# Optimization experiments

Hardware: AMD Instinct MI355X
Metric: run time of the kernel (lower is better)

## Reference

```python
import jax, jax.numpy as jnp
import numpy as np

N_ATOMS = 200000   # total atoms in batch
N_NBR   = 10       # max neighbors per atom (a2a width)
N_MOLS  = 8000     # molecules in batch (25 atoms each)
HID     = 128      # hidden_size
FDIM    = 151      # raw atom feature dim (GROVER default)
FEAT    = 200      # molecule-level descriptor dim
DFF     = 4 * HID  # PositionwiseFeedForward inner dim
FFN_H   = 256      # mol_atom_from_atom_ffn hidden
TASKS   = 12       # num_tasks
EPS     = 1e-6     # GROVER LayerNorm eps


def setup_inputs() -> dict:
    key = jax.random.key(0)
    ks = jax.random.split(key, 14)
    s = 0.02
    atoms_per_mol = N_ATOMS // N_MOLS
    starts = (jnp.arange(N_MOLS, dtype=jnp.int32) * atoms_per_mol)
    sizes = jnp.full((N_MOLS,), atoms_per_mol, dtype=jnp.int32)
    a_scope = jnp.stack([starts, sizes], axis=1)  # [M, 2]
    return {
        "atom_output": jax.random.normal(ks[0], (N_ATOMS, HID), jnp.float32),
        "original_f_atoms": jax.random.normal(ks[1], (N_ATOMS, FDIM), jnp.float32),
        "features_batch": jax.random.normal(ks[2], (N_MOLS, FEAT), jnp.float32),
        "a2a": jax.random.randint(ks[3], (N_ATOMS, N_NBR), 0, N_ATOMS, jnp.int32),
        "a_scope": a_scope,
        # PositionwiseFeedForward (ffn_atom_from_atom): in = FDIM + HID
        "W1": jax.random.normal(ks[4], (FDIM + HID, DFF), jnp.float32) * s,
        "b1": jnp.zeros((DFF,), jnp.float32),
        "W2": jax.random.normal(ks[5], (DFF, HID), jnp.float32) * s,
        "b2": jnp.zeros((HID,), jnp.float32),
        # SublayerConnection LayerNorm
        "gamma": jnp.ones((HID,), jnp.float32),
        "beta": jnp.zeros((HID,), jnp.float32),
        # mol_atom_from_atom_ffn: in = HID + FEAT
        "Wf1": jax.random.normal(ks[6], (HID + FEAT, FFN_H), jnp.float32) * s,
        "bf1": jnp.zeros((FFN_H,), jnp.float32),
        "Wf2": jax.random.normal(ks[7], (FFN_H, TASKS), jnp.float32) * s,
        "bf2": jnp.zeros((TASKS,), jnp.float32),
    }


def _layernorm(x, gamma, beta):
    mu = jnp.mean(x, axis=-1, keepdims=True)
    var = jnp.mean((x - mu) ** 2, axis=-1, keepdims=True)
    return gamma * (x - mu) * jax.lax.rsqrt(var + EPS) + beta


def reference(atom_output, original_f_atoms, features_batch, a2a, a_scope,
              W1, b1, W2, b2, gamma, beta, Wf1, bf1, Wf2, bf2):
    # select_neighbor_and_aggregate: gather neighbor embeddings, sum over nbrs
    aggr = jnp.sum(atom_output[a2a], axis=1)                      # [N, HID]
    x = jnp.concatenate([original_f_atoms, aggr], axis=1)         # [N, FDIM+HID]
    # PositionwiseFeedForward (eval: dropout = identity)
    h = jax.nn.relu(x @ W1 + b1)
    ffn_out = h @ W2 + b2                                         # [N, HID]
    # SublayerConnection(None, x) -> dropout(LayerNorm(x))
    atom_emb = _layernorm(ffn_out, gamma, beta)                   # [N, HID]
    # Readout: mean-pool per molecule via a_scope (start, size)
    starts = a_scope[:, 0]
    sizes = a_scope[:, 1].astype(atom_emb.dtype)
    seg = jnp.searchsorted(starts, jnp.arange(atom_emb.shape[0], dtype=starts.dtype), side="right") - 1
    mol = jax.ops.segment_sum(atom_emb, seg, num_segments=a_scope.shape[0]) / sizes[:, None]
    # concat molecule descriptors, then mol_atom_from_atom_ffn
    mol = jnp.concatenate([mol, features_batch], axis=1)          # [M, HID+FEAT]
    out = jax.nn.relu(mol @ Wf1 + bf1) @ Wf2 + bf2                # [M, TASKS]
    return out
```

## Files before the change

kernel.cpp:

```cpp
#include <hip/hip_runtime.h>
#include <hip/hip_bf16.h>

#define N_ATOMS 200000
#define N_NBR 10
#define N_MOLS 8000
#define HID 128
#define FDIM 151
#define FEAT 200
#define DFF 512
#define FFN_H 256
#define TASKS 12
#define KX 279
#define K1P 288
#define XS 296
#define HSTR 136
#define FS 132
#define KM 328
#define K3 352
#define MS 360
#define MT 80
#define MI 5
#define NCHUNK 4
#define SMEM_ATOMS (MT * XS * 2 + MT * HSTR * 2)

typedef __hip_bfloat16 bf16;
typedef __attribute__((ext_vector_type(8))) __bf16 bf16x8;
typedef __attribute__((ext_vector_type(4))) float f32x4;

__device__ __forceinline__ float bf2f(bf16 x) { return __bfloat162float(x); }
__device__ __forceinline__ float blo(unsigned w) { union { unsigned u; float f; } c; c.u = w << 16; return c.f; }
__device__ __forceinline__ float bhi(unsigned w) { union { unsigned u; float f; } c; c.u = w & 0xFFFF0000u; return c.f; }

__global__ void prep_weights_kernel(const float* __restrict__ W1,
                                    const float* __restrict__ W2,
                                    const float* __restrict__ Wf1,
                                    bf16* __restrict__ W1bT,
                                    bf16* __restrict__ W2bT,
                                    bf16* __restrict__ Wf1bT) {
  int idx = blockIdx.x * 256 + threadIdx.x;
  if (idx < DFF * K1P) {
    int n = idx / K1P, k = idx - n * K1P;
    float v;
    if (k < HID)      v = W1[(size_t)(FDIM + k) * DFF + n];
    else if (k < KX)  v = W1[(size_t)(k - HID) * DFF + n];
    else              v = 0.f;
    W1bT[idx] = __float2bfloat16(v);
    return;
  }
  idx -= DFF * K1P;
  if (idx < HID * DFF) {
    int n = idx / DFF, k = idx - n * DFF;
    W2bT[idx] = __float2bfloat16(W2[(size_t)k * HID + n]);
    return;
  }
  idx -= HID * DFF;
  if (idx < FFN_H * K3) {
    int n = idx / K3, k = idx - n * K3;
    float v = (k < KM) ? Wf1[(size_t)k * FFN_H + n] : 0.f;
    Wf1bT[idx] = __float2bfloat16(v);
  }
}

__global__ void conv_ao_kernel(const float* __restrict__ ao, bf16* __restrict__ ao16) {
  const int idx = blockIdx.x * 256 + threadIdx.x;
  const float4 v0 = *(const float4*)&ao[(size_t)idx * 8];
  const float4 v1 = *(const float4*)&ao[(size_t)idx * 8 + 4];
  union { bf16 h[8]; uint4 u; } pk;
  pk.h[0] = __float2bfloat16(v0.x); pk.h[1] = __float2bfloat16(v0.y);
  pk.h[2] = __float2bfloat16(v0.z); pk.h[3] = __float2bfloat16(v0.w);
  pk.h[4] = __float2bfloat16(v1.x); pk.h[5] = __float2bfloat16(v1.y);
  pk.h[6] = __float2bfloat16(v1.z); pk.h[7] = __float2bfloat16(v1.w);
  *(uint4*)&ao16[(size_t)idx * 8] = pk.u;
}

__global__ __launch_bounds__(256)
void gather_kernel(const bf16* __restrict__ ao16,
                   const int* __restrict__ a2a,
                   bf16* __restrict__ aggr) {
  const int gid = blockIdx.x * 256 + threadIdx.x;
  const int atom = gid >> 4, c8 = gid & 15;
  int idxs[N_NBR];
#pragma unroll
  for (int j = 0; j < N_NBR; ++j) idxs[j] = a2a[atom * N_NBR + j];
  float s[8];
#pragma unroll
  for (int e = 0; e < 8; ++e) s[e] = 0.f;
#pragma unroll
  for (int j = 0; j < N_NBR; ++j) {
    const uint4 u = *(const uint4*)&ao16[(size_t)idxs[j] * HID + c8 * 8];
    s[0] += blo(u.x); s[1] += bhi(u.x);
    s[2] += blo(u.y); s[3] += bhi(u.y);
    s[4] += blo(u.z); s[5] += bhi(u.z);
    s[6] += blo(u.w); s[7] += bhi(u.w);
  }
  union { bf16 h[8]; uint4 u; } pk;
#pragma unroll
  for (int e = 0; e < 8; ++e) pk.h[e] = __float2bfloat16(s[e]);
  *(uint4*)&aggr[(size_t)atom * HID + c8 * 8] = pk.u;
}

__global__ __launch_bounds__(512, 4)
void atoms_kernel(const bf16* __restrict__ aggr,
                  const float* __restrict__ f_atoms,
                  const bf16* __restrict__ W1bT,
                  const float* __restrict__ b1,
                  const bf16* __restrict__ W2bT,
                  const float* __restrict__ b2,
                  const float* __restrict__ gamma,
                  const float* __restrict__ beta,
                  bf16* __restrict__ atom_emb) {
  extern __shared__ char smem[];
  bf16* Xs = (bf16*)smem;
  bf16* Hs = (bf16*)(smem + MT * XS * 2);
  float* Fs = (float*)smem;

  const int tid = threadIdx.x;
  const int m0 = blockIdx.x * MT;
  const int lane = tid & 63;
  const int w = tid >> 6;
  const int lr = lane & 15;
  const int lk = lane >> 4;

  const float4 b2v = *(const float4*)&b2[w * 16 + lk * 4];
  const float gam0 = gamma[lane], gam1 = gamma[64 + lane];
  const float bet0 = beta[lane],  bet1 = beta[64 + lane];

  {
    int q = tid;
#pragma unroll
    for (int p = 0; p < 3; ++p) {
      if (p < 2 || q < MT * 16) {
        const int r = q >> 4, c8 = q & 15;
        *(uint4*)&Xs[r * XS + c8 * 8] = *(const uint4*)&aggr[(size_t)(m0 + r) * HID + c8 * 8];
      }
      q += 512;
    }
  }
  {
    const float* fb = &f_atoms[(size_t)m0 * FDIM];
    int q = tid;
#pragma unroll
    for (int p = 0; p < 6; ++p) {
      if (p < 5 || q < (MT * FDIM) / 4) {
        const float4 v = *(const float4*)&fb[q * 4];
        const float vf[4] = { v.x, v.y, v.z, v.w };
        const int flat = q * 4;
        const int r0 = flat / FDIM, c0 = flat - r0 * FDIM;
#pragma unroll
        for (int e = 0; e < 4; ++e) {
          const int cc = c0 + e;
          const int off = (cc < FDIM) ? (r0 * XS + HID + cc) : ((r0 + 1) * XS + HID + cc - FDIM);
          Xs[off] = __float2bfloat16(vf[e]);
        }
      }
      q += 512;
    }
  }
  {
    int q = tid;
#pragma unroll
    for (int p = 0; p < 2; ++p) {
      if (q < MT * (K1P - KX)) {
        const int r = q / (K1P - KX), cc = q - r * (K1P - KX);
        Xs[r * XS + KX + cc] = __float2bfloat16(0.f);
      }
      q += 512;
    }
  }
  __syncthreads();

  f32x4 acc2[MI];
#pragma unroll
  for (int mi = 0; mi < MI; ++mi) acc2[mi] = (f32x4)0.f;

#pragma unroll 1
  for (int nc = 0; nc < NCHUNK; ++nc) {
    f32x4 acc1[MI];
#pragma unroll
    for (int mi = 0; mi < MI; ++mi) acc1[mi] = (f32x4)0.f;
    const bf16* w1row = &W1bT[(size_t)(nc * 128 + w * 16 + lr) * K1P + lk * 8];
    __builtin_amdgcn_s_setprio(1);
#pragma unroll
    for (int kk = 0; kk < K1P / 32; ++kk) {
      const bf16x8 b = *(const bf16x8*)&w1row[kk * 32];
#pragma unroll
      for (int mi = 0; mi < MI; ++mi) {
        const bf16x8 a = *(const bf16x8*)&Xs[(mi * 16 + lr) * XS + kk * 32 + lk * 8];
        acc1[mi] = __builtin_amdgcn_mfma_f32_16x16x32_bf16(b, a, acc1[mi], 0, 0, 0);
      }
    }
    __builtin_amdgcn_s_setprio(0);
    {
      const float4 bb = *(const float4*)&b1[nc * 128 + w * 16 + lk * 4];
      const float bbf[4] = { bb.x, bb.y, bb.z, bb.w };
      const int nb4 = w * 16 + lk * 4;
#pragma unroll
      for (int mi = 0; mi < MI; ++mi) {
        union { bf16 h[4]; uint2 u2; } pk;
#pragma unroll
        for (int r = 0; r < 4; ++r) {
          const float h = acc1[mi][r] + bbf[r];
          pk.h[r] = __float2bfloat16(h > 0.f ? h : 0.f);
        }
        *(uint2*)&Hs[(mi * 16 + lr) * HSTR + nb4] = pk.u2;
      }
    }
    __syncthreads();

    const bf16* w2row = &W2bT[(size_t)(w * 16 + lr) * DFF + nc * 128 + lk * 8];
    __builtin_amdgcn_s_setprio(1);
#pragma unroll
    for (int kk = 0; kk < 4; ++kk) {
      const bf16x8 b = *(const bf16x8*)&w2row[kk * 32];
#pragma unroll
      for (int mi = 0; mi < MI; ++mi) {
        const bf16x8 a = *(const bf16x8*)&Hs[(mi * 16 + lr) * HSTR + kk * 32 + lk * 8];
        acc2[mi] = __builtin_amdgcn_mfma_f32_16x16x32_bf16(b, a, acc2[mi], 0, 0, 0);
      }
    }
    __builtin_amdgcn_s_setprio(0);
    if (nc < NCHUNK - 1) __syncthreads();
  }

  {
    const int nb4 = w * 16 + lk * 4;
#pragma unroll
    for (int mi = 0; mi < MI; ++mi) {
      float4 v;
      v.x = acc2[mi][0] + b2v.x;
      v.y = acc2[mi][1] + b2v.y;
      v.z = acc2[mi][2] + b2v.z;
      v.w = acc2[mi][3] + b2v.w;
      *(float4*)&Fs[(mi * 16 + lr) * FS + nb4] = v;
    }
  }
  __syncthreads();

#pragma unroll
  for (int i = 0; i < MT / 8; ++i) {
    const int row = w * (MT / 8) + i;
    const float x0 = Fs[row * FS + lane];
    const float x1 = Fs[row * FS + 64 + lane];
    float s = x0 + x1;
    float q = x0 * x0 + x1 * x1;
#pragma unroll
    for (int off = 32; off > 0; off >>= 1) {
      s += __shfl_xor(s, off);
      q += __shfl_xor(q, off);
    }
    const float mu = s * (1.f / 128.f);
    const float var = q * (1.f / 128.f) - mu * mu;
    const float rs = rsqrtf(var + 1e-6f);
    const int atom = m0 + row;
    atom_emb[(size_t)atom * HID + lane] =
        __float2bfloat16(gam0 * ((x0 - mu) * rs) + bet0);
    atom_emb[(size_t)atom * HID + 64 + lane] =
        __float2bfloat16(gam1 * ((x1 - mu) * rs) + bet1);
  }
}

__global__ __launch_bounds__(256)
void mol_kernel(const bf16* __restrict__ atom_emb,
                const float* __restrict__ features,
                const int* __restrict__ a_scope,
                bf16* __restrict__ mol_cat) {
  const int tid = threadIdx.x;
  const int mi = tid >> 4, c8 = tid & 15;
  const int base = blockIdx.x * 16;
  const int m = base + mi;
  const int start = a_scope[2 * m];
  const int size  = a_scope[2 * m + 1];
  float s[8];
#pragma unroll
  for (int e = 0; e < 8; ++e) s[e] = 0.f;
  for (int a = 0; a < size; ++a) {
    const uint4 u = *(const uint4*)&atom_emb[(size_t)(start + a) * HID + c8 * 8];
    s[0] += blo(u.x); s[1] += bhi(u.x);
    s[2] += blo(u.y); s[3] += bhi(u.y);
    s[4] += blo(u.z); s[5] += bhi(u.z);
    s[6] += blo(u.w); s[7] += bhi(u.w);
  }
  const float inv = 1.f / (float)size;
  union { bf16 h[8]; uint4 u; } pk;
#pragma unroll
  for (int e = 0; e < 8; ++e) pk.h[e] = __float2bfloat16(s[e] * inv);
  *(uint4*)&mol_cat[(size_t)m * K3 + c8 * 8] = pk.u;
  for (int q = tid; q < 16 * 50; q += 256) {
    const int mm = q / 50, qq = q - mm * 50;
    const float4 v = *(const float4*)&features[(size_t)(base + mm) * FEAT + qq * 4];
    union { bf16 h[4]; uint2 u2; } pf;
    pf.h[0] = __float2bfloat16(v.x); pf.h[1] = __float2bfloat16(v.y);
    pf.h[2] = __float2bfloat16(v.z); pf.h[3] = __float2bfloat16(v.w);
    *(uint2*)&mol_cat[(size_t)(base + mm) * K3 + HID + qq * 4] = pf.u2;
  }
  for (int q = tid; q < 16 * (K3 - KM); q += 256) {
    const int mm = q / (K3 - KM), qq = q - mm * (K3 - KM);
    mol_cat[(size_t)(base + mm) * K3 + KM + qq] = __float2bfloat16(0.f);
  }
}

__global__ __launch_bounds__(512)
void molffn1_kernel(const bf16* __restrict__ mol_cat,
                    const bf16* __restrict__ Wf1bT,
                    const float* __restrict__ bf1,
                    bf16* __restrict__ Hf) {
  __shared__ bf16 As[64 * MS];
  const int tid = threadIdx.x;
  const int m0 = blockIdx.x * 64;
  for (int idx = tid; idx < 64 * (K3 / 8); idx += 512) {
    int rr = idx / (K3 / 8), qv = idx - rr * (K3 / 8);
    *(uint4*)&As[rr * MS + qv * 8] = *(const uint4*)&mol_cat[(size_t)(m0 + rr) * K3 + qv * 8];
  }
  __syncthreads();
  const int lane = tid & 63, w = tid >> 6;
  const int lr = lane & 15, lk = lane >> 4;
  const int wn = w * 32;
  f32x4 acc[4][2];
#pragma unroll
  for (int mi = 0; mi < 4; ++mi)
#pragma unroll
    for (int ni = 0; ni < 2; ++ni) acc[mi][ni] = (f32x4)0.f;
#pragma unroll 3
  for (int kk = 0; kk < K3 / 32; ++kk) {
    bf16x8 a[4], b[2];
#pragma unroll
    for (int mi = 0; mi < 4; ++mi)
      a[mi] = *(const bf16x8*)&As[(mi * 16 + lr) * MS + kk * 32 + lk * 8];
#pragma unroll
    for (int ni = 0; ni < 2; ++ni)
      b[ni] = *(const bf16x8*)&Wf1bT[(size_t)(wn + ni * 16 + lr) * K3 + kk * 32 + lk * 8];
#pragma unroll
    for (int mi = 0; mi < 4; ++mi)
#pragma unroll
      for (int ni = 0; ni < 2; ++ni)
        acc[mi][ni] = __builtin_amdgcn_mfma_f32_16x16x32_bf16(a[mi], b[ni], acc[mi][ni], 0, 0, 0);
  }
#pragma unroll
  for (int ni = 0; ni < 2; ++ni) {
    const int n = wn + ni * 16 + lr;
    const float bias = bf1[n];
#pragma unroll
    for (int mi = 0; mi < 4; ++mi)
#pragma unroll
      for (int rr = 0; rr < 4; ++rr) {
        const int row = mi * 16 + lk * 4 + rr;
        const float h = acc[mi][ni][rr] + bias;
        Hf[(size_t)(m0 + row) * FFN_H + n] = __float2bfloat16(h > 0.f ? h : 0.f);
      }
  }
}

__global__ __launch_bounds__(192)
void molffn2_kernel(const bf16* __restrict__ Hf,
                    const float* __restrict__ Wf2,
                    const float* __restrict__ bias2,
                    float* __restrict__ out) {
  __shared__ float Ws[FFN_H * TASKS];
  const int tid = threadIdx.x;
  for (int i = tid; i < FFN_H * TASKS; i += 192) Ws[i] = Wf2[i];
  __syncthreads();
  const int m = blockIdx.x * 16 + tid / TASKS;
  const int t = tid % TASKS;
  float s = bias2[t];
  for (int k8 = 0; k8 < FFN_H / 8; ++k8) {
    const uint4 u = *(const uint4*)&Hf[(size_t)m * FFN_H + k8 * 8];
    const float h[8] = { blo(u.x), bhi(u.x), blo(u.y), bhi(u.y),
                         blo(u.z), bhi(u.z), blo(u.w), bhi(u.w) };
#pragma unroll
    for (int e = 0; e < 8; ++e) s += h[e] * Ws[(k8 * 8 + e) * TASKS + t];
  }
  out[(size_t)m * TASKS + t] = s;
}

extern "C" void kernel_launch(void* const* d_in, const int* in_sizes, int n_in,
                              void* d_out, int out_size, void* d_ws, size_t ws_size,
                              hipStream_t stream) {
  const float* atom_output = (const float*)d_in[0];
  const float* f_atoms     = (const float*)d_in[1];
  const float* features    = (const float*)d_in[2];
  const int*   a2a         = (const int*)d_in[3];
  const int*   a_scope     = (const int*)d_in[4];
  const float* W1   = (const float*)d_in[5];
  const float* b1   = (const float*)d_in[6];
  const float* W2   = (const float*)d_in[7];
  const float* b2   = (const float*)d_in[8];
  const float* gamma = (const float*)d_in[9];
  const float* beta  = (const float*)d_in[10];
  const float* Wf1  = (const float*)d_in[11];
  const float* bf1  = (const float*)d_in[12];
  const float* Wf2  = (const float*)d_in[13];
  const float* bf2v = (const float*)d_in[14];
  float* out = (float*)d_out;

  char* ws = (char*)d_ws;
  size_t off = 0;
  bf16* W1bT  = (bf16*)(ws + off); off += (size_t)DFF * K1P * 2;
  bf16* W2bT  = (bf16*)(ws + off); off += (size_t)HID * DFF * 2;
  bf16* Wf1bT = (bf16*)(ws + off); off += (size_t)FFN_H * K3 * 2;
  bf16* atom_emb = (bf16*)(ws + off); off += (size_t)N_ATOMS * HID * 2;
  bf16* mol_cat  = (bf16*)(ws + off); off += (size_t)N_MOLS * K3 * 2;
  bf16* Hf       = (bf16*)(ws + off); off += (size_t)N_MOLS * FFN_H * 2;
  bf16* ao16     = (bf16*)(ws + off); off += (size_t)N_ATOMS * HID * 2;
  bf16* aggr = atom_emb;

  static int smem_set = 0;
  (void)smem_set;
  hipFuncSetAttribute((const void*)atoms_kernel,
                      hipFuncAttributeMaxDynamicSharedMemorySize, SMEM_ATOMS);

  hipLaunchKernelGGL(prep_weights_kernel, dim3(1184), dim3(256), 0, stream,
                     W1, W2, Wf1, W1bT, W2bT, Wf1bT);
  hipLaunchKernelGGL(conv_ao_kernel, dim3(N_ATOMS * HID / 8 / 256), dim3(256), 0, stream,
                     atom_output, ao16);
  hipLaunchKernelGGL(gather_kernel, dim3(N_ATOMS * 16 / 256), dim3(256), 0, stream,
                     ao16, a2a, aggr);
  hipLaunchKernelGGL(atoms_kernel, dim3(N_ATOMS / MT), dim3(512), SMEM_ATOMS, stream,
                     aggr, f_atoms,
                     W1bT, b1, W2bT, b2, gamma, beta, atom_emb);
  hipLaunchKernelGGL(mol_kernel, dim3(N_MOLS / 16), dim3(256), 0, stream,
                     atom_emb, features, a_scope, mol_cat);
  hipLaunchKernelGGL(molffn1_kernel, dim3(N_MOLS / 64), dim3(512), 0, stream,
                     mol_cat, Wf1bT, bf1, Hf);
  hipLaunchKernelGGL(molffn2_kernel, dim3(N_MOLS / 16), dim3(192), 0, stream,
                     Hf, Wf2, bf2v, out);
}
```

Measured before the change: 285.6 us.

## Retile atom FFN kernel to 2x4 warp tiles with 64-row blocks

Changes the fused atom FFN kernel from 80-row tiles, where each warp owns a 16-column strip across all rows, to 64-row tiles with a 2x4 warp grid. Each warp now computes a 32x64 block of the first GEMM and a 32x32 block of the second GEMM, processing DFF in two 256-wide chunks instead of four 128-wide chunks. The aim is more register-level reuse of A and B fragments (several MFMAs per load), fewer weight reloads from global memory, and fewer barriers. In exchange the kernel uses more accumulator registers, which may lower occupancy, and launches more blocks because each block covers fewer rows.

```diff
diff --git a/kernel.cpp b/kernel.cpp
--- a/kernel.cpp
+++ b/kernel.cpp
@@ -13,15 +13,14 @@
 #define KX 279
 #define K1P 288
 #define XS 296
-#define HSTR 136
+#define HS2 264
 #define FS 132
 #define KM 328
 #define K3 352
 #define MS 360
-#define MT 80
-#define MI 5
-#define NCHUNK 4
-#define SMEM_ATOMS (MT * XS * 2 + MT * HSTR * 2)
+#define MT 64
+#define NC 256
+#define SMEM_ATOMS (MT * XS * 2 + MT * HS2 * 2)
 
 typedef __hip_bfloat16 bf16;
 typedef __attribute__((ext_vector_type(8))) __bf16 bf16x8;
@@ -120,19 +119,18 @@
   const int w = tid >> 6;
   const int lr = lane & 15;
   const int lk = lane >> 4;
-
-  const float4 b2v = *(const float4*)&b2[w * 16 + lk * 4];
+  const int wm = w & 1;
+  const int wq = w >> 1;
+
   const float gam0 = gamma[lane], gam1 = gamma[64 + lane];
   const float bet0 = beta[lane],  bet1 = beta[64 + lane];
 
   {
     int q = tid;
 #pragma unroll
-    for (int p = 0; p < 3; ++p) {
-      if (p < 2 || q < MT * 16) {
-        const int r = q >> 4, c8 = q & 15;
-        *(uint4*)&Xs[r * XS + c8 * 8] = *(const uint4*)&aggr[(size_t)(m0 + r) * HID + c8 * 8];
-      }
+    for (int p = 0; p < 2; ++p) {
+      const int r = q >> 4, c8 = q & 15;
+      *(uint4*)&Xs[r * XS + c8 * 8] = *(const uint4*)&aggr[(size_t)(m0 + r) * HID + c8 * 8];
       q += 512;
     }
   }
@@ -140,8 +138,8 @@
     const float* fb = &f_atoms[(size_t)m0 * FDIM];
     int q = tid;
 #pragma unroll
-    for (int p = 0; p < 6; ++p) {
-      if (p < 5 || q < (MT * FDIM) / 4) {
+    for (int p = 0; p < 5; ++p) {
+      if (p < 4 || q < (MT * FDIM) / 4) {
         const float4 v = *(const float4*)&fb[q * 4];
         const float vf[4] = { v.x, v.y, v.z, v.w };
         const int flat = q * 4;
@@ -156,82 +154,94 @@
       q += 512;
     }
   }
-  {
-    int q = tid;
-#pragma unroll
-    for (int p = 0; p < 2; ++p) {
-      if (q < MT * (K1P - KX)) {
-        const int r = q / (K1P - KX), cc = q - r * (K1P - KX);
-        Xs[r * XS + KX + cc] = __float2bfloat16(0.f);
+  if (tid < MT * (K1P - KX)) {
+    const int r = tid / (K1P - KX), cc = tid - r * (K1P - KX);
+    Xs[r * XS + KX + cc] = __float2bfloat16(0.f);
+  }
+  __syncthreads();
+
+  f32x4 acc2[2][2];
+#pragma unroll
+  for (int mi = 0; mi < 2; ++mi)
+#pragma unroll
+    for (int ni = 0; ni < 2; ++ni) acc2[mi][ni] = (f32x4)0.f;
+
+#pragma unroll 1
+  for (int nc = 0; nc < 2; ++nc) {
+    {
+      f32x4 acc1[2][4];
+#pragma unroll
+      for (int mi = 0; mi < 2; ++mi)
+#pragma unroll
+        for (int ni = 0; ni < 4; ++ni) acc1[mi][ni] = (f32x4)0.f;
+      const bf16* w1p = &W1bT[(size_t)(nc * NC + wq * 64 + lr) * K1P + lk * 8];
+      __builtin_amdgcn_s_setprio(1);
+#pragma unroll
+      for (int kk = 0; kk < K1P / 32; ++kk) {
+        bf16x8 b[4], a[2];
+#pragma unroll
+        for (int ni = 0; ni < 4; ++ni)
+          b[ni] = *(const bf16x8*)&w1p[(size_t)ni * 16 * K1P + kk * 32];
+#pragma unroll
+        for (int mi = 0; mi < 2; ++mi)
+          a[mi] = *(const bf16x8*)&Xs[(wm * 32 + mi * 16 + lr) * XS + kk * 32 + lk * 8];
+#pragma unroll
+        for (int mi = 0; mi < 2; ++mi)
+#pragma unroll
+          for (int ni = 0; ni < 4; ++ni)
+            acc1[mi][ni] = __builtin_amdgcn_mfma_f32_16x16x32_bf16(b[ni], a[mi], acc1[mi][ni], 0, 0, 0);
       }
-      q += 512;
-    }
-  }
-  __syncthreads();
-
-  f32x4 acc2[MI];
-#pragma unroll
-  for (int mi = 0; mi < MI; ++mi) acc2[mi] = (f32x4)0.f;
-
-#pragma unroll 1
-  for (int nc = 0; nc < NCHUNK; ++nc) {
-    f32x4 acc1[MI];
-#pragma unroll
-    for (int mi = 0; mi < MI; ++mi) acc1[mi] = (f32x4)0.f;
-    const bf16* w1row = &W1bT[(size_t)(nc * 128 + w * 16 + lr) * K1P + lk * 8];
+      __builtin_amdgcn_s_setprio(0);
+#pragma unroll
+      for (int ni = 0; ni < 4; ++ni) {
+        const float4 bb = *(const float4*)&b1[nc * NC + wq * 64 + ni * 16 + lk * 4];
+        const float bbf[4] = { bb.x, bb.y, bb.z, bb.w };
+        const int nloc = wq * 64 + ni * 16 + lk * 4;
+#pragma unroll
+        for (int mi = 0; mi < 2; ++mi) {
+          union { bf16 h[4]; uint2 u2; } pk;
+#pragma unroll
+          for (int r = 0; r < 4; ++r) {
+            const float h = acc1[mi][ni][r] + bbf[r];
+            pk.h[r] = __float2bfloat16(h > 0.f ? h : 0.f);
+          }
+          *(uint2*)&Hs[(wm * 32 + mi * 16 + lr) * HS2 + nloc] = pk.u2;
+        }
+      }
+    }
+    __syncthreads();
+
     __builtin_amdgcn_s_setprio(1);
 #pragma unroll
-    for (int kk = 0; kk < K1P / 32; ++kk) {
-      const bf16x8 b = *(const bf16x8*)&w1row[kk * 32];
-#pragma unroll
-      for (int mi = 0; mi < MI; ++mi) {
-        const bf16x8 a = *(const bf16x8*)&Xs[(mi * 16 + lr) * XS + kk * 32 + lk * 8];
-        acc1[mi] = __builtin_amdgcn_mfma_f32_16x16x32_bf16(b, a, acc1[mi], 0, 0, 0);
-      }
+    for (int kk = 0; kk < NC / 32; ++kk) {
+      bf16x8 wb[2], hb[2];
+#pragma unroll
+      for (int ni = 0; ni < 2; ++ni)
+        wb[ni] = *(const bf16x8*)&W2bT[(size_t)(wq * 32 + ni * 16 + lr) * DFF + nc * NC + kk * 32 + lk * 8];
+#pragma unroll
+      for (int mi = 0; mi < 2; ++mi)
+        hb[mi] = *(const bf16x8*)&Hs[(wm * 32 + mi * 16 + lr) * HS2 + kk * 32 + lk * 8];
+#pragma unroll
+      for (int mi = 0; mi < 2; ++mi)
+#pragma unroll
+        for (int ni = 0; ni < 2; ++ni)
+          acc2[mi][ni] = __builtin_amdgcn_mfma_f32_16x16x32_bf16(wb[ni], hb[mi], acc2[mi][ni], 0, 0, 0);
     }
     __builtin_amdgcn_s_setprio(0);
-    {
-      const float4 bb = *(const float4*)&b1[nc * 128 + w * 16 + lk * 4];
-      const float bbf[4] = { bb.x, bb.y, bb.z, bb.w };
-      const int nb4 = w * 16 + lk * 4;
-#pragma unroll
-      for (int mi = 0; mi < MI; ++mi) {
-        union { bf16 h[4]; uint2 u2; } pk;
-#pragma unroll
-        for (int r = 0; r < 4; ++r) {
-          const float h = acc1[mi][r] + bbf[r];
-          pk.h[r] = __float2bfloat16(h > 0.f ? h : 0.f);
-        }
-        *(uint2*)&Hs[(mi * 16 + lr) * HSTR + nb4] = pk.u2;
-      }
-    }
-    __syncthreads();
-
-    const bf16* w2row = &W2bT[(size_t)(w * 16 + lr) * DFF + nc * 128 + lk * 8];
-    __builtin_amdgcn_s_setprio(1);
-#pragma unroll
-    for (int kk = 0; kk < 4; ++kk) {
-      const bf16x8 b = *(const bf16x8*)&w2row[kk * 32];
-#pragma unroll
-      for (int mi = 0; mi < MI; ++mi) {
-        const bf16x8 a = *(const bf16x8*)&Hs[(mi * 16 + lr) * HSTR + kk * 32 + lk * 8];
-        acc2[mi] = __builtin_amdgcn_mfma_f32_16x16x32_bf16(b, a, acc2[mi], 0, 0, 0);
-      }
-    }
-    __builtin_amdgcn_s_setprio(0);
-    if (nc < NCHUNK - 1) __syncthreads();
-  }
-
-  {
-    const int nb4 = w * 16 + lk * 4;
-#pragma unroll
-    for (int mi = 0; mi < MI; ++mi) {
+    if (nc == 0) __syncthreads();
+  }
+
+#pragma unroll
+  for (int ni = 0; ni < 2; ++ni) {
+    const float4 bb = *(const float4*)&b2[wq * 32 + ni * 16 + lk * 4];
+#pragma unroll
+    for (int mi = 0; mi < 2; ++mi) {
       float4 v;
-      v.x = acc2[mi][0] + b2v.x;
-      v.y = acc2[mi][1] + b2v.y;
-      v.z = acc2[mi][2] + b2v.z;
-      v.w = acc2[mi][3] + b2v.w;
-      *(float4*)&Fs[(mi * 16 + lr) * FS + nb4] = v;
+      v.x = acc2[mi][ni][0] + bb.x;
+      v.y = acc2[mi][ni][1] + bb.y;
+      v.z = acc2[mi][ni][2] + bb.z;
+      v.w = acc2[mi][ni][3] + bb.w;
+      *(float4*)&Fs[(wm * 32 + mi * 16 + lr) * FS + wq * 32 + ni * 16 + lk * 4] = v;
     }
   }
   __syncthreads();
@@ -403,8 +413,6 @@
   bf16* ao16     = (bf16*)(ws + off); off += (size_t)N_ATOMS * HID * 2;
   bf16* aggr = atom_emb;
 
-  static int smem_set = 0;
-  (void)smem_set;
   hipFuncSetAttribute((const void*)atoms_kernel,
                       hipFuncAttributeMaxDynamicSharedMemorySize, SMEM_ATOMS);
 
```

New measurement: 381.3 us. 33.5% more time.

## Precompute bf16 atom features and restructure atom FFN with double-buffered hidden tiles

Applied to the files above, without the earlier changes.

A new kernel converts the fp32 atom features to a padded bf16 buffer, replacing the per-element scalar conversion inside the atom FFN kernel with vector copies. The FFN kernel now uses 64-atom tiles and computes all four first-GEMM chunks in one pass, so each LDS load of the input tile is reused across every output chunk. The second GEMM runs over double-buffered hidden tiles, writing the next chunk's ReLU output while the current one is consumed. The cost is an extra kernel launch plus a round trip of the converted features through memory, and the 16 accumulator tiles sit under a 512x4 launch bound, which may force register spills.

```diff
diff --git a/kernel.cpp b/kernel.cpp
--- a/kernel.cpp
+++ b/kernel.cpp
@@ -18,10 +18,9 @@
 #define KM 328
 #define K3 352
 #define MS 360
-#define MT 80
-#define MI 5
-#define NCHUNK 4
-#define SMEM_ATOMS (MT * XS * 2 + MT * HSTR * 2)
+#define MT 64
+#define XFC 152
+#define SMEM_ATOMS (MT * XS * 2 + 2 * MT * HSTR * 2)
 
 typedef __hip_bfloat16 bf16;
 typedef __attribute__((ext_vector_type(8))) __bf16 bf16x8;
@@ -99,9 +98,25 @@
   *(uint4*)&aggr[(size_t)atom * HID + c8 * 8] = pk.u;
 }
 
+__global__ __launch_bounds__(256)
+void conv_fa_kernel(const float* __restrict__ f_atoms, bf16* __restrict__ Xf) {
+  const int gid = blockIdx.x * 256 + threadIdx.x;
+  if (gid >= N_ATOMS * 19) return;
+  const int atom = gid / 19, o8 = gid - (gid / 19) * 19;
+  const float* src = &f_atoms[(size_t)atom * FDIM + o8 * 8];
+  const int rem = FDIM - o8 * 8;
+  union { bf16 h[8]; uint4 u; } pk;
+#pragma unroll
+  for (int e = 0; e < 8; ++e) {
+    const float v = (e < rem) ? src[e] : 0.f;
+    pk.h[e] = __float2bfloat16(v);
+  }
+  *(uint4*)&Xf[(size_t)atom * XFC + o8 * 8] = pk.u;
+}
+
 __global__ __launch_bounds__(512, 4)
 void atoms_kernel(const bf16* __restrict__ aggr,
-                  const float* __restrict__ f_atoms,
+                  const bf16* __restrict__ Xf,
                   const bf16* __restrict__ W1bT,
                   const float* __restrict__ b1,
                   const bf16* __restrict__ W2bT,
@@ -110,8 +125,9 @@
                   const float* __restrict__ beta,
                   bf16* __restrict__ atom_emb) {
   extern __shared__ char smem[];
-  bf16* Xs = (bf16*)smem;
-  bf16* Hs = (bf16*)(smem + MT * XS * 2);
+  bf16* Xs  = (bf16*)smem;
+  bf16* Hs0 = (bf16*)(smem + MT * XS * 2);
+  bf16* Hs1 = Hs0 + MT * HSTR;
   float* Fs = (float*)smem;
 
   const int tid = threadIdx.x;
@@ -121,117 +137,104 @@
   const int lr = lane & 15;
   const int lk = lane >> 4;
 
-  const float4 b2v = *(const float4*)&b2[w * 16 + lk * 4];
   const float gam0 = gamma[lane], gam1 = gamma[64 + lane];
   const float bet0 = beta[lane],  bet1 = beta[64 + lane];
 
   {
     int q = tid;
 #pragma unroll
-    for (int p = 0; p < 3; ++p) {
-      if (p < 2 || q < MT * 16) {
-        const int r = q >> 4, c8 = q & 15;
-        *(uint4*)&Xs[r * XS + c8 * 8] = *(const uint4*)&aggr[(size_t)(m0 + r) * HID + c8 * 8];
+    for (int p = 0; p < 2; ++p) {
+      const int r = q >> 4, c8 = q & 15;
+      *(uint4*)&Xs[r * XS + c8 * 8] = *(const uint4*)&aggr[(size_t)(m0 + r) * HID + c8 * 8];
+      q += 512;
+    }
+  }
+  for (int q = tid; q < MT * 19; q += 512) {
+    const int r = q / 19, o = q - (q / 19) * 19;
+    *(uint4*)&Xs[r * XS + HID + o * 8] = *(const uint4*)&Xf[(size_t)(m0 + r) * XFC + o * 8];
+  }
+  if (tid < MT) {
+    const uint4 z = {0u, 0u, 0u, 0u};
+    *(uint4*)&Xs[tid * XS + 280] = z;
+  }
+  __syncthreads();
+
+  f32x4 acc1[4][4];
+#pragma unroll
+  for (int nc = 0; nc < 4; ++nc)
+#pragma unroll
+    for (int mi = 0; mi < 4; ++mi) acc1[nc][mi] = (f32x4)0.f;
+  {
+    const bf16* w1base = &W1bT[(size_t)(w * 16 + lr) * K1P + lk * 8];
+    __builtin_amdgcn_s_setprio(1);
+#pragma unroll 3
+    for (int kk = 0; kk < K1P / 32; ++kk) {
+      bf16x8 a[4];
+#pragma unroll
+      for (int mi = 0; mi < 4; ++mi)
+        a[mi] = *(const bf16x8*)&Xs[(mi * 16 + lr) * XS + kk * 32 + lk * 8];
+#pragma unroll
+      for (int nc = 0; nc < 4; ++nc) {
+        const bf16x8 b = *(const bf16x8*)&w1base[(size_t)nc * 128 * K1P + kk * 32];
+#pragma unroll
+        for (int mi = 0; mi < 4; ++mi)
+          acc1[nc][mi] = __builtin_amdgcn_mfma_f32_16x16x32_bf16(b, a[mi], acc1[nc][mi], 0, 0, 0);
       }
-      q += 512;
-    }
-  }
+    }
+    __builtin_amdgcn_s_setprio(0);
+  }
+
+  auto epi = [&](int nc, bf16* Hb) {
+    const float4 bb = *(const float4*)&b1[nc * 128 + w * 16 + lk * 4];
+    const float bbf[4] = { bb.x, bb.y, bb.z, bb.w };
+#pragma unroll
+    for (int mi = 0; mi < 4; ++mi) {
+      union { bf16 h[4]; uint2 u2; } pk;
+#pragma unroll
+      for (int r = 0; r < 4; ++r) {
+        const float h = acc1[nc][mi][r] + bbf[r];
+        pk.h[r] = __float2bfloat16(h > 0.f ? h : 0.f);
+      }
+      *(uint2*)&Hb[(mi * 16 + lr) * HSTR + w * 16 + lk * 4] = pk.u2;
+    }
+  };
+
+  epi(0, Hs0);
+  __syncthreads();
+
+  f32x4 acc2[4];
+#pragma unroll
+  for (int mi = 0; mi < 4; ++mi) acc2[mi] = (f32x4)0.f;
+
+#pragma unroll
+  for (int nc = 0; nc < 4; ++nc) {
+    bf16* cur = (nc & 1) ? Hs1 : Hs0;
+    if (nc < 3) epi(nc + 1, (nc & 1) ? Hs0 : Hs1);
+    const bf16* w2p = &W2bT[(size_t)(w * 16 + lr) * DFF + nc * 128 + lk * 8];
+    __builtin_amdgcn_s_setprio(1);
+#pragma unroll
+    for (int kk = 0; kk < 4; ++kk) {
+      const bf16x8 wb = *(const bf16x8*)&w2p[kk * 32];
+#pragma unroll
+      for (int mi = 0; mi < 4; ++mi) {
+        const bf16x8 hb = *(const bf16x8*)&cur[(mi * 16 + lr) * HSTR + kk * 32 + lk * 8];
+        acc2[mi] = __builtin_amdgcn_mfma_f32_16x16x32_bf16(wb, hb, acc2[mi], 0, 0, 0);
+      }
+    }
+    __builtin_amdgcn_s_setprio(0);
+    __syncthreads();
+  }
+
   {
-    const float* fb = &f_atoms[(size_t)m0 * FDIM];
-    int q = tid;
-#pragma unroll
-    for (int p = 0; p < 6; ++p) {
-      if (p < 5 || q < (MT * FDIM) / 4) {
-        const float4 v = *(const float4*)&fb[q * 4];
-        const float vf[4] = { v.x, v.y, v.z, v.w };
-        const int flat = q * 4;
-        const int r0 = flat / FDIM, c0 = flat - r0 * FDIM;
-#pragma unroll
-        for (int e = 0; e < 4; ++e) {
-          const int cc = c0 + e;
-          const int off = (cc < FDIM) ? (r0 * XS + HID + cc) : ((r0 + 1) * XS + HID + cc - FDIM);
-          Xs[off] = __float2bfloat16(vf[e]);
-        }
-      }
-      q += 512;
-    }
-  }
-  {
-    int q = tid;
-#pragma unroll
-    for (int p = 0; p < 2; ++p) {
-      if (q < MT * (K1P - KX)) {
-        const int r = q / (K1P - KX), cc = q - r * (K1P - KX);
-        Xs[r * XS + KX + cc] = __float2bfloat16(0.f);
-      }
-      q += 512;
-    }
-  }
-  __syncthreads();
-
-  f32x4 acc2[MI];
-#pragma unroll
-  for (int mi = 0; mi < MI; ++mi) acc2[mi] = (f32x4)0.f;
-
-#pragma unroll 1
-  for (int nc = 0; nc < NCHUNK; ++nc) {
-    f32x4 acc1[MI];
-#pragma unroll
-    for (int mi = 0; mi < MI; ++mi) acc1[mi] = (f32x4)0.f;
-    const bf16* w1row = &W1bT[(size_t)(nc * 128 + w * 16 + lr) * K1P + lk * 8];
-    __builtin_amdgcn_s_setprio(1);
-#pragma unroll
-    for (int kk = 0; kk < K1P / 32; ++kk) {
-      const bf16x8 b = *(const bf16x8*)&w1row[kk * 32];
-#pragma unroll
-      for (int mi = 0; mi < MI; ++mi) {
-        const bf16x8 a = *(const bf16x8*)&Xs[(mi * 16 + lr) * XS + kk * 32 + lk * 8];
-        acc1[mi] = __builtin_amdgcn_mfma_f32_16x16x32_bf16(b, a, acc1[mi], 0, 0, 0);
-      }
-    }
-    __builtin_amdgcn_s_setprio(0);
-    {
-      const float4 bb = *(const float4*)&b1[nc * 128 + w * 16 + lk * 4];
-      const float bbf[4] = { bb.x, bb.y, bb.z, bb.w };
-      const int nb4 = w * 16 + lk * 4;
-#pragma unroll
-      for (int mi = 0; mi < MI; ++mi) {
-        union { bf16 h[4]; uint2 u2; } pk;
-#pragma unroll
-        for (int r = 0; r < 4; ++r) {
-          const float h = acc1[mi][r] + bbf[r];
-          pk.h[r] = __float2bfloat16(h > 0.f ? h : 0.f);
-        }
-        *(uint2*)&Hs[(mi * 16 + lr) * HSTR + nb4] = pk.u2;
-      }
-    }
-    __syncthreads();
-
-    const bf16* w2row = &W2bT[(size_t)(w * 16 + lr) * DFF + nc * 128 + lk * 8];
-    __builtin_amdgcn_s_setprio(1);
-#pragma unroll
-    for (int kk = 0; kk < 4; ++kk) {
-      const bf16x8 b = *(const bf16x8*)&w2row[kk * 32];
-#pragma unroll
-      for (int mi = 0; mi < MI; ++mi) {
-        const bf16x8 a = *(const bf16x8*)&Hs[(mi * 16 + lr) * HSTR + kk * 32 + lk * 8];
-        acc2[mi] = __builtin_amdgcn_mfma_f32_16x16x32_bf16(b, a, acc2[mi], 0, 0, 0);
-      }
-    }
-    __builtin_amdgcn_s_setprio(0);
-    if (nc < NCHUNK - 1) __syncthreads();
-  }
-
-  {
-    const int nb4 = w * 16 + lk * 4;
-#pragma unroll
-    for (int mi = 0; mi < MI; ++mi) {
+    const float4 b2v = *(const float4*)&b2[w * 16 + lk * 4];
+#pragma unroll
+    for (int mi = 0; mi < 4; ++mi) {
       float4 v;
       v.x = acc2[mi][0] + b2v.x;
       v.y = acc2[mi][1] + b2v.y;
       v.z = acc2[mi][2] + b2v.z;
       v.w = acc2[mi][3] + b2v.w;
-      *(float4*)&Fs[(mi * 16 + lr) * FS + nb4] = v;
+      *(float4*)&Fs[(mi * 16 + lr) * FS + w * 16 + lk * 4] = v;
     }
   }
   __syncthreads();
@@ -398,13 +401,14 @@
   bf16* W2bT  = (bf16*)(ws + off); off += (size_t)HID * DFF * 2;
   bf16* Wf1bT = (bf16*)(ws + off); off += (size_t)FFN_H * K3 * 2;
   bf16* atom_emb = (bf16*)(ws + off); off += (size_t)N_ATOMS * HID * 2;
-  bf16* mol_cat  = (bf16*)(ws + off); off += (size_t)N_MOLS * K3 * 2;
-  bf16* Hf       = (bf16*)(ws + off); off += (size_t)N_MOLS * FFN_H * 2;
-  bf16* ao16     = (bf16*)(ws + off); off += (size_t)N_ATOMS * HID * 2;
+  char* regionR = ws + off;
+  bf16* ao16    = (bf16*)regionR;
+  bf16* mol_cat = (bf16*)(regionR + (size_t)N_ATOMS * HID * 2);
+  bf16* Hf      = (bf16*)(regionR + (size_t)N_ATOMS * HID * 2
+                                   + (size_t)N_MOLS * K3 * 2);
+  bf16* Xf      = (bf16*)regionR;
   bf16* aggr = atom_emb;
 
-  static int smem_set = 0;
-  (void)smem_set;
   hipFuncSetAttribute((const void*)atoms_kernel,
                       hipFuncAttributeMaxDynamicSharedMemorySize, SMEM_ATOMS);
 
@@ -414,8 +418,10 @@
                      atom_output, ao16);
   hipLaunchKernelGGL(gather_kernel, dim3(N_ATOMS * 16 / 256), dim3(256), 0, stream,
                      ao16, a2a, aggr);
+  hipLaunchKernelGGL(conv_fa_kernel, dim3((N_ATOMS * 19 + 255) / 256), dim3(256), 0, stream,
+                     f_atoms, Xf);
   hipLaunchKernelGGL(atoms_kernel, dim3(N_ATOMS / MT), dim3(512), SMEM_ATOMS, stream,
-                     aggr, f_atoms,
+                     aggr, Xf,
                      W1bT, b1, W2bT, b2, gamma, beta, atom_emb);
   hipLaunchKernelGGL(mol_kernel, dim3(N_MOLS / 16), dim3(256), 0, stream,
                      atom_emb, features, a_scope, mol_cat);
```

After: 352.8 us. 23.5% more time.

## Shrink atom tile to 64, XOR-swizzle LDS, process two DFF chunks per pass

Applied to the files above, without the earlier changes.

The atoms kernel tile drops from 80 to 64 rows, and the padded LDS strides are replaced by unpadded rows with XOR swizzling to avoid bank conflicts. The first GEMM now computes two 128-wide DFF chunks per pass, so each A fragment read from LDS feeds two MFMAs. LDS becomes static and launch bounds rise to 6 blocks per CU, aiming for more occupancy and fewer LDS reads. In exchange there are more blocks, more accumulator registers, and an extra barrier per chunk.

```diff
diff --git a/kernel.cpp b/kernel.cpp
--- a/kernel.cpp
+++ b/kernel.cpp
@@ -12,16 +12,14 @@
 #define TASKS 12
 #define KX 279
 #define K1P 288
-#define XS 296
-#define HSTR 136
+#define XSB 288
+#define HSB 128
 #define FS 132
 #define KM 328
 #define K3 352
 #define MS 360
-#define MT 80
-#define MI 5
-#define NCHUNK 4
-#define SMEM_ATOMS (MT * XS * 2 + MT * HSTR * 2)
+#define MT 64
+#define SMEM_ATOMS (MT * XSB * 2 + MT * HSB * 2)
 
 typedef __hip_bfloat16 bf16;
 typedef __attribute__((ext_vector_type(8))) __bf16 bf16x8;
@@ -30,6 +28,13 @@
 __device__ __forceinline__ float bf2f(bf16 x) { return __bfloat162float(x); }
 __device__ __forceinline__ float blo(unsigned w) { union { unsigned u; float f; } c; c.u = w << 16; return c.f; }
 __device__ __forceinline__ float bhi(unsigned w) { union { unsigned u; float f; } c; c.u = w & 0xFFFF0000u; return c.f; }
+
+__device__ __forceinline__ int xswz(int r, int e) {
+  return r * XSB + (e ^ ((e < 256 ? (r & 7) : (r & 3)) << 3));
+}
+__device__ __forceinline__ int hswz(int r, int e) {
+  return r * HSB + (e ^ ((r & 7) << 3));
+}
 
 __global__ void prep_weights_kernel(const float* __restrict__ W1,
                                     const float* __restrict__ W2,
@@ -99,7 +104,7 @@
   *(uint4*)&aggr[(size_t)atom * HID + c8 * 8] = pk.u;
 }
 
-__global__ __launch_bounds__(512, 4)
+__global__ __launch_bounds__(512, 6)
 void atoms_kernel(const bf16* __restrict__ aggr,
                   const float* __restrict__ f_atoms,
                   const bf16* __restrict__ W1bT,
@@ -109,9 +114,9 @@
                   const float* __restrict__ gamma,
                   const float* __restrict__ beta,
                   bf16* __restrict__ atom_emb) {
-  extern __shared__ char smem[];
+  __shared__ char smem[SMEM_ATOMS];
   bf16* Xs = (bf16*)smem;
-  bf16* Hs = (bf16*)(smem + MT * XS * 2);
+  bf16* Hs = (bf16*)(smem + MT * XSB * 2);
   float* Fs = (float*)smem;
 
   const int tid = threadIdx.x;
@@ -121,18 +126,13 @@
   const int lr = lane & 15;
   const int lk = lane >> 4;
 
-  const float4 b2v = *(const float4*)&b2[w * 16 + lk * 4];
-  const float gam0 = gamma[lane], gam1 = gamma[64 + lane];
-  const float bet0 = beta[lane],  bet1 = beta[64 + lane];
-
   {
     int q = tid;
 #pragma unroll
-    for (int p = 0; p < 3; ++p) {
-      if (p < 2 || q < MT * 16) {
-        const int r = q >> 4, c8 = q & 15;
-        *(uint4*)&Xs[r * XS + c8 * 8] = *(const uint4*)&aggr[(size_t)(m0 + r) * HID + c8 * 8];
-      }
+    for (int p = 0; p < 2; ++p) {
+      const int r = q >> 4, c8 = q & 15;
+      *(uint4*)&Xs[r * XSB + ((c8 * 8) ^ ((r & 7) << 3))] =
+          *(const uint4*)&aggr[(size_t)(m0 + r) * HID + c8 * 8];
       q += 512;
     }
   }
@@ -140,8 +140,8 @@
     const float* fb = &f_atoms[(size_t)m0 * FDIM];
     int q = tid;
 #pragma unroll
-    for (int p = 0; p < 6; ++p) {
-      if (p < 5 || q < (MT * FDIM) / 4) {
+    for (int p = 0; p < 5; ++p) {
+      if (p < 4 || q < (MT * FDIM) / 4) {
         const float4 v = *(const float4*)&fb[q * 4];
         const float vf[4] = { v.x, v.y, v.z, v.w };
         const int flat = q * 4;
@@ -149,93 +149,100 @@
 #pragma unroll
         for (int e = 0; e < 4; ++e) {
           const int cc = c0 + e;
-          const int off = (cc < FDIM) ? (r0 * XS + HID + cc) : ((r0 + 1) * XS + HID + cc - FDIM);
-          Xs[off] = __float2bfloat16(vf[e]);
+          const int rr = (cc < FDIM) ? r0 : r0 + 1;
+          const int ee = HID + ((cc < FDIM) ? cc : cc - FDIM);
+          Xs[xswz(rr, ee)] = __float2bfloat16(vf[e]);
         }
       }
       q += 512;
     }
   }
+  if (tid < MT * (K1P - KX)) {
+    const int r = tid / (K1P - KX), cc = tid - r * (K1P - KX);
+    Xs[xswz(r, KX + cc)] = __float2bfloat16(0.f);
+  }
+  __syncthreads();
+
+  f32x4 acc2[4];
+#pragma unroll
+  for (int mi = 0; mi < 4; ++mi) acc2[mi] = (f32x4)0.f;
+
+#pragma unroll 1
+  for (int pp = 0; pp < 2; ++pp) {
+    const int c0 = pp * 2;
+    f32x4 acc1[2][4];
+#pragma unroll
+    for (int c = 0; c < 2; ++c)
+#pragma unroll
+      for (int mi = 0; mi < 4; ++mi) acc1[c][mi] = (f32x4)0.f;
+    {
+      const bf16* w1p = &W1bT[(size_t)(c0 * 128 + w * 16 + lr) * K1P + lk * 8];
+      __builtin_amdgcn_s_setprio(1);
+#pragma unroll
+      for (int kk = 0; kk < K1P / 32; ++kk) {
+        bf16x8 b0 = *(const bf16x8*)&w1p[kk * 32];
+        bf16x8 b1f = *(const bf16x8*)&w1p[(size_t)128 * K1P + kk * 32];
+#pragma unroll
+        for (int mi = 0; mi < 4; ++mi) {
+          const bf16x8 a = *(const bf16x8*)&Xs[xswz(mi * 16 + lr, kk * 32 + lk * 8)];
+          acc1[0][mi] = __builtin_amdgcn_mfma_f32_16x16x32_bf16(b0, a, acc1[0][mi], 0, 0, 0);
+          acc1[1][mi] = __builtin_amdgcn_mfma_f32_16x16x32_bf16(b1f, a, acc1[1][mi], 0, 0, 0);
+        }
+      }
+      __builtin_amdgcn_s_setprio(0);
+    }
+#pragma unroll
+    for (int c = 0; c < 2; ++c) {
+      const int nc = c0 + c;
+      {
+        const float4 bb = *(const float4*)&b1[nc * 128 + w * 16 + lk * 4];
+        const float bbf[4] = { bb.x, bb.y, bb.z, bb.w };
+#pragma unroll
+        for (int mi = 0; mi < 4; ++mi) {
+          union { bf16 h[4]; uint2 u2; } pk;
+#pragma unroll
+          for (int r = 0; r < 4; ++r) {
+            const float h = acc1[c][mi][r] + bbf[r];
+            pk.h[r] = __float2bfloat16(h > 0.f ? h : 0.f);
+          }
+          *(uint2*)&Hs[hswz(mi * 16 + lr, w * 16 + lk * 4)] = pk.u2;
+        }
+      }
+      __syncthreads();
+      {
+        const bf16* w2p = &W2bT[(size_t)(w * 16 + lr) * DFF + nc * 128 + lk * 8];
+        __builtin_amdgcn_s_setprio(1);
+#pragma unroll
+        for (int kk = 0; kk < 4; ++kk) {
+          const bf16x8 wb = *(const bf16x8*)&w2p[kk * 32];
+#pragma unroll
+          for (int mi = 0; mi < 4; ++mi) {
+            const bf16x8 hb = *(const bf16x8*)&Hs[hswz(mi * 16 + lr, kk * 32 + lk * 8)];
+            acc2[mi] = __builtin_amdgcn_mfma_f32_16x16x32_bf16(wb, hb, acc2[mi], 0, 0, 0);
+          }
+        }
+        __builtin_amdgcn_s_setprio(0);
+      }
+      __syncthreads();
+    }
+  }
+
   {
-    int q = tid;
-#pragma unroll
-    for (int p = 0; p < 2; ++p) {
-      if (q < MT * (K1P - KX)) {
-        const int r = q / (K1P - KX), cc = q - r * (K1P - KX);
-        Xs[r * XS + KX + cc] = __float2bfloat16(0.f);
-      }
-      q += 512;
-    }
-  }
-  __syncthreads();
-
-  f32x4 acc2[MI];
-#pragma unroll
-  for (int mi = 0; mi < MI; ++mi) acc2[mi] = (f32x4)0.f;
-
-#pragma unroll 1
-  for (int nc = 0; nc < NCHUNK; ++nc) {
-    f32x4 acc1[MI];
-#pragma unroll
-    for (int mi = 0; mi < MI; ++mi) acc1[mi] = (f32x4)0.f;
-    const bf16* w1row = &W1bT[(size_t)(nc * 128 + w * 16 + lr) * K1P + lk * 8];
-    __builtin_amdgcn_s_setprio(1);
-#pragma unroll
-    for (int kk = 0; kk < K1P / 32; ++kk) {
-      const bf16x8 b = *(const bf16x8*)&w1row[kk * 32];
-#pragma unroll
-      for (int mi = 0; mi < MI; ++mi) {
-        const bf16x8 a = *(const bf16x8*)&Xs[(mi * 16 + lr) * XS + kk * 32 + lk * 8];
-        acc1[mi] = __builtin_amdgcn_mfma_f32_16x16x32_bf16(b, a, acc1[mi], 0, 0, 0);
-      }
-    }
-    __builtin_amdgcn_s_setprio(0);
-    {
-      const float4 bb = *(const float4*)&b1[nc * 128 + w * 16 + lk * 4];
-      const float bbf[4] = { bb.x, bb.y, bb.z, bb.w };
-      const int nb4 = w * 16 + lk * 4;
-#pragma unroll
-      for (int mi = 0; mi < MI; ++mi) {
-        union { bf16 h[4]; uint2 u2; } pk;
-#pragma unroll
-        for (int r = 0; r < 4; ++r) {
-          const float h = acc1[mi][r] + bbf[r];
-          pk.h[r] = __float2bfloat16(h > 0.f ? h : 0.f);
-        }
-        *(uint2*)&Hs[(mi * 16 + lr) * HSTR + nb4] = pk.u2;
-      }
-    }
-    __syncthreads();
-
-    const bf16* w2row = &W2bT[(size_t)(w * 16 + lr) * DFF + nc * 128 + lk * 8];
-    __builtin_amdgcn_s_setprio(1);
-#pragma unroll
-    for (int kk = 0; kk < 4; ++kk) {
-      const bf16x8 b = *(const bf16x8*)&w2row[kk * 32];
-#pragma unroll
-      for (int mi = 0; mi < MI; ++mi) {
-        const bf16x8 a = *(const bf16x8*)&Hs[(mi * 16 + lr) * HSTR + kk * 32 + lk * 8];
-        acc2[mi] = __builtin_amdgcn_mfma_f32_16x16x32_bf16(b, a, acc2[mi], 0, 0, 0);
-      }
-    }
-    __builtin_amdgcn_s_setprio(0);
-    if (nc < NCHUNK - 1) __syncthreads();
-  }
-
-  {
-    const int nb4 = w * 16 + lk * 4;
-#pragma unroll
-    for (int mi = 0; mi < MI; ++mi) {
+    const float4 b2v = *(const float4*)&b2[w * 16 + lk * 4];
+#pragma unroll
+    for (int mi = 0; mi < 4; ++mi) {
       float4 v;
       v.x = acc2[mi][0] + b2v.x;
       v.y = acc2[mi][1] + b2v.y;
       v.z = acc2[mi][2] + b2v.z;
       v.w = acc2[mi][3] + b2v.w;
-      *(float4*)&Fs[(mi * 16 + lr) * FS + nb4] = v;
+      *(float4*)&Fs[(mi * 16 + lr) * FS + w * 16 + lk * 4] = v;
     }
   }
   __syncthreads();
 
+  const float gam0 = gamma[lane], gam1 = gamma[64 + lane];
+  const float bet0 = beta[lane],  bet1 = beta[64 + lane];
 #pragma unroll
   for (int i = 0; i < MT / 8; ++i) {
     const int row = w * (MT / 8) + i;
@@ -403,18 +410,13 @@
   bf16* ao16     = (bf16*)(ws + off); off += (size_t)N_ATOMS * HID * 2;
   bf16* aggr = atom_emb;
 
-  static int smem_set = 0;
-  (void)smem_set;
-  hipFuncSetAttribute((const void*)atoms_kernel,
-                      hipFuncAttributeMaxDynamicSharedMemorySize, SMEM_ATOMS);
-
   hipLaunchKernelGGL(prep_weights_kernel, dim3(1184), dim3(256), 0, stream,
                      W1, W2, Wf1, W1bT, W2bT, Wf1bT);
   hipLaunchKernelGGL(conv_ao_kernel, dim3(N_ATOMS * HID / 8 / 256), dim3(256), 0, stream,
                      atom_output, ao16);
   hipLaunchKernelGGL(gather_kernel, dim3(N_ATOMS * 16 / 256), dim3(256), 0, stream,
                      ao16, a2a, aggr);
-  hipLaunchKernelGGL(atoms_kernel, dim3(N_ATOMS / MT), dim3(512), SMEM_ATOMS, stream,
+  hipLaunchKernelGGL(atoms_kernel, dim3(N_ATOMS / MT), dim3(512), 0, stream,
                      aggr, f_atoms,
                      W1bT, b1, W2bT, b2, gamma, beta, atom_emb);
   hipLaunchKernelGGL(mol_kernel, dim3(N_MOLS / 16), dim3(256), 0, stream,
```

Result: slower. 318.5 us (+11.5%).
